# Optimization experiments

Measured on AMD Instinct MI355X. Metric: run time of the kernel, lower is better.

Reference implementation:

```python
import jax, jax.numpy as jnp
import numpy as np
import math
from jax.scipy.linalg import cho_solve

B, N, HD, H, M = 8, 2048, 512, 8, 128
VD = HD // H          # per-head dim = 64
LAM = 0.01            # lambda_noise
EPS = 0.002           # cgp_eps


def setup_inputs() -> dict:
    key = jax.random.key(0)
    ks = jax.random.split(key, 10)
    def lin(k):
        return jax.random.normal(k, (HD, HD), jnp.float32) * 0.01  # init std=0.01
    z = jnp.zeros((HD,), jnp.float32)
    return {
        "x": jax.random.normal(ks[0], (B, N, HD), jnp.float32),
        "input_mask": jnp.ones((B, N), jnp.float32),
        "Wq": lin(ks[1]), "bq": z,
        "Wk": lin(ks[2]), "bk": z,
        "Wv": lin(ks[3]), "bv": z,
        "Wx0": lin(ks[4]), "bx0": z,
        "Wo": lin(ks[5]), "bo": z,
        "omega": jax.random.normal(ks[6], (VD, M), jnp.float32),  # lengthscale=1.0
        "b_rff": 2.0 * math.pi * jax.random.uniform(ks[7], (M,), jnp.float32),
        "cur_k": 0,
    }


def _forward(x, input_mask, Wq, bq, Wk, bk, Wv, bv, Wx0, bx0, Wo, bo, omega, b_rff):
    Bb, Nn, hd = x.shape
    mask = input_mask.astype(x.dtype)
    mN = mask[:, None, :, None]                         # [B,1,N,1]

    def heads(W, bias):
        return (x @ W.T + bias).reshape(Bb, Nn, H, VD).transpose(0, 2, 1, 3)  # [B,H,N,vd]

    q = heads(Wq, bq)
    k = heads(Wk, bk)
    v = heads(Wv, bv) * mN
    x0 = heads(Wx0, bx0)

    scale = jnp.sqrt(jnp.asarray(2.0 / M, x.dtype))
    def rff(X):
        Z = jnp.einsum('bhnd,dm->bhnm', X, omega) + b_rff
        return scale * jnp.cos(Z)

    Phi_q = rff(q) * mN   # [B,H,N,m]
    Phi_k = rff(k) * mN
    Phi_o = rff(x0) * mN

    I = jnp.eye(M, dtype=x.dtype)
    Gk = jnp.einsum('bhnm,bhnp->bhmp', Phi_k, Phi_k)    # [B,H,m,m]
    Go = jnp.einsum('bhnm,bhnp->bhmp', Phi_o, Phi_o)
    Ak = Gk + LAM * I
    Ao = Go + LAM * I
    Lk = jnp.linalg.cholesky(Ak)
    Lo = jnp.linalg.cholesky(Ao)

    PkTv = jnp.einsum('bhnm,bhnd->bhmd', Phi_k, v)      # [B,H,m,vd]
    Akinv_PkTv = cho_solve((Lk, True), PkTv)
    proj = jnp.einsum('bhnm,bhmd->bhnd', Phi_k, Akinv_PkTv)
    u = (v - proj) / LAM

    Ieb = jnp.broadcast_to(I, Ao.shape)
    Ao_inv = cho_solve((Lo, True), Ieb)                 # [B,H,m,m]
    B_o = Go @ Ao_inv
    PkTu = jnp.einsum('bhnm,bhnd->bhmd', Phi_k, u)
    mid = B_o @ PkTu
    y = jnp.einsum('bhnm,bhmd->bhnd', Phi_q, mid)       # [B,H,N,vd]

    out = y.transpose(0, 2, 1, 3).reshape(Bb, Nn, hd)[:, None]  # [B,1,N,hdim]
    out = out @ Wo.T + bo

    # ---- _cgp_lower_bounds(Phi_q, Phi_k, Phi_o, v) ----
    # A = Go + lam*I == Ao (reuse Lo, Ao_inv); Ck == Gk.
    D = VD
    Cq = jnp.einsum('bhnm,bhnp->bhmp', Phi_q, Phi_q)
    Ck = Gk
    S_q = Ao / LAM + Cq / EPS
    S_k = Ao / LAM + Ck / EPS
    S_q_inv = cho_solve((jnp.linalg.cholesky(S_q), True), Ieb)
    S_k_inv = cho_solve((jnp.linalg.cholesky(S_k), True), Ieb)

    G_Ainv = Go @ Ao_inv
    const = Nn * math.log(2 * math.pi)

    # q-branch
    yy = jnp.sum(v * v, axis=(2, 3))
    PhiT_y = jnp.einsum('bhnm,bhnd->bhmd', Phi_q, v)
    Sq_inv_PhiT_y = S_q_inv @ PhiT_y
    datafit_q = yy / EPS - jnp.sum(PhiT_y * Sq_inv_PhiT_y, axis=(2, 3)) / (EPS * EPS)
    M_q = Cq / EPS - (Cq @ S_q_inv @ Cq) / (EPS * EPS)
    model_q = D * jnp.einsum('bhmn,bhmn->bh', G_Ainv, M_q)
    Iadd_q = I + (LAM / EPS) * (Ao_inv @ Cq)
    logdet_q = Nn * math.log(EPS) + jnp.linalg.slogdet(Iadd_q)[1]
    LB_q = -0.5 * (datafit_q + model_q + logdet_q + const)

    # k-branch
    tr_Ck = jnp.trace(Ck, axis1=-2, axis2=-1)
    tr_part = jnp.trace(S_k_inv @ (Ck @ Ck), axis1=-2, axis2=-1)
    datafit_k = D * (tr_Ck / EPS - tr_part / (EPS * EPS))
    M_k = Ck / EPS - (Ck @ S_k_inv @ Ck) / (EPS * EPS)
    model_k = D * jnp.einsum('bhmn,bhmn->bh', G_Ainv, M_k)
    Iadd_k = I + (LAM / EPS) * (Ao_inv @ Ck)
    logdet_k = Nn * math.log(EPS) + jnp.linalg.slogdet(Iadd_k)[1]
    LB_k = -0.5 * (datafit_k + model_k + logdet_k + const)

    reg = -(LB_q + LB_k).mean()
    return out, reg


def reference(x, input_mask, Wq, bq, Wk, bk, Wv, bv, Wx0, bx0, Wo, bo, omega, b_rff, cur_k):
    return _forward(x, input_mask, Wq, bq, Wk, bk, Wv, bv, Wx0, bx0, Wo, bo, omega, b_rff)
```

## Files before the change

### kernel.cpp

```cpp
#include <hip/hip_runtime.h>
#include <math.h>

#define B_ 8
#define N_ 2048
#define HD_ 512
#define H_ 8
#define M_ 128
#define VD_ 64

typedef __attribute__((ext_vector_type(8))) short short8v;
typedef __attribute__((ext_vector_type(4))) float f32x4;

__device__ __forceinline__ unsigned short f2bf(float f) {
  unsigned u = __float_as_uint(f);
  u += 0x7FFF + ((u >> 16) & 1);
  return (unsigned short)(u >> 16);
}
__device__ __forceinline__ float bf2f(unsigned short h) {
  return __uint_as_float(((unsigned)h) << 16);
}

__global__ __launch_bounds__(256) void split_kernel(
    const float* __restrict__ in, unsigned short* __restrict__ hi,
    unsigned short* __restrict__ lo, int n)
{
  const int i = (blockIdx.x * 256 + threadIdx.x) << 2;
  if (i >= n) return;
  float4 v = *(const float4*)(in + i);
  ushort4 h, l;
  h.x = f2bf(v.x); l.x = f2bf(v.x - bf2f(h.x));
  h.y = f2bf(v.y); l.y = f2bf(v.y - bf2f(h.y));
  h.z = f2bf(v.z); l.z = f2bf(v.z - bf2f(h.z));
  h.w = f2bf(v.w); l.w = f2bf(v.w - bf2f(h.w));
  *(ushort4*)(hi + i) = h;
  *(ushort4*)(lo + i) = l;
}

__global__ __launch_bounds__(256) void womb_kernel(
    const float* __restrict__ Wq, const float* __restrict__ Wk, const float* __restrict__ Wx0,
    const float* __restrict__ bq, const float* __restrict__ bk, const float* __restrict__ bx0,
    const float* __restrict__ omega, const float* __restrict__ brff,
    unsigned short* __restrict__ WOmH, unsigned short* __restrict__ WOmL,
    float* __restrict__ bias2)
{
  const int blk = blockIdx.x, tid = threadIdx.x;
  const int path = blk >> 10, hm = blk & 1023;
  const int h = hm >> 7, m = hm & 127;
  const float* W  = (path == 0) ? Wq : (path == 1) ? Wk : Wx0;
  const float* bv = (path == 0) ? bq : (path == 1) ? bk : bx0;
  __shared__ float om[64];
  if (tid < 64) om[tid] = omega[tid * 128 + m];
  __syncthreads();
  for (int c = tid; c < 512; c += 256) {
    float s = 0.f;
#pragma unroll 8
    for (int d = 0; d < 64; ++d) s = fmaf(W[(h * 64 + d) * 512 + c], om[d], s);
    const unsigned short sh = f2bf(s);
    const size_t o = (size_t)(path * 1024 + hm) * 512 + c;
    WOmH[o] = sh;
    WOmL[o] = f2bf(s - bf2f(sh));
  }
  if (tid == 0) {
    float s = 0.f;
    for (int d = 0; d < 64; ++d) s = fmaf(bv[h * 64 + d], om[d], s);
    bias2[path * 1024 + hm] = s + brff[m];
  }
}

#define LDP 40
#define GEMM_PROLOGUE(NCOLBITS)                                              \
  __shared__ unsigned short Ah[128 * LDP], Al[128 * LDP];                    \
  __shared__ unsigned short Bh[128 * LDP], Bl[128 * LDP];                    \
  const int tid = threadIdx.x;                                               \
  const int bx = blockIdx.x & ((1 << (NCOLBITS)) - 1);                       \
  const int by = blockIdx.x >> (NCOLBITS);                                   \
  const int row0 = by << 7, col0 = bx << 7;                                  \
  const int lane = tid & 63, wave = tid >> 6;                                \
  const int wr = wave >> 1, wc = wave & 1;                                   \
  const int fr = lane & 15, fk = (lane >> 4) << 3;                           \
  f32x4 acc[4][4];                                                           \
  _Pragma("unroll") for (int i = 0; i < 4; ++i)                              \
  _Pragma("unroll") for (int j = 0; j < 4; ++j)                              \
      acc[i][j] = (f32x4){0.f, 0.f, 0.f, 0.f};                               \
  const int srow = tid >> 2;                                                 \
  const int sch = (tid & 3) << 3;                                            \
  const size_t ga = (size_t)(row0 + srow) * 512 + sch;                       \
  const size_t gb = (size_t)(col0 + srow) * 512 + sch;                       \
  short8v rah0, rah1, ral0, ral1, rbh0, rbh1, rbl0, rbl1;

#define LOADREGS(k)                                                          \
  rah0 = *(const short8v*)(Ahi + ga + (k));                                  \
  rah1 = *(const short8v*)(Ahi + ga + (size_t)64 * 512 + (k));               \
  ral0 = *(const short8v*)(Alo + ga + (k));                                  \
  ral1 = *(const short8v*)(Alo + ga + (size_t)64 * 512 + (k));               \
  rbh0 = *(const short8v*)(Bhi + gb + (k));                                  \
  rbh1 = *(const short8v*)(Bhi + gb + (size_t)64 * 512 + (k));               \
  rbl0 = *(const short8v*)(Blo + gb + (k));                                  \
  rbl1 = *(const short8v*)(Blo + gb + (size_t)64 * 512 + (k));

#define GEMM_KLOOP                                                           \
  LOADREGS(0)                                                                \
  for (int kt = 0; kt < 16; ++kt) {                                          \
    __syncthreads();                                                         \
    *(short8v*)&Ah[srow * LDP + sch] = rah0;                                 \
    *(short8v*)&Ah[(srow + 64) * LDP + sch] = rah1;                          \
    *(short8v*)&Al[srow * LDP + sch] = ral0;                                 \
    *(short8v*)&Al[(srow + 64) * LDP + sch] = ral1;                          \
    *(short8v*)&Bh[srow * LDP + sch] = rbh0;                                 \
    *(short8v*)&Bh[(srow + 64) * LDP + sch] = rbh1;                          \
    *(short8v*)&Bl[srow * LDP + sch] = rbl0;                                 \
    *(short8v*)&Bl[(srow + 64) * LDP + sch] = rbl1;                          \
    __syncthreads();                                                         \
    if (kt < 15) { LOADREGS((kt + 1) * 32) }                                 \
    short8v a_hi[4], a_lo[4];                                                \
    _Pragma("unroll") for (int i = 0; i < 4; ++i) {                          \
      const int ar = (wr * 64 + i * 16 + fr) * LDP + fk;                     \
      a_hi[i] = *(const short8v*)&Ah[ar];                                    \
      a_lo[i] = *(const short8v*)&Al[ar];                                    \
    }                                                                        \
    _Pragma("unroll") for (int j = 0; j < 4; ++j) {                          \
      const int br = (wc * 64 + j * 16 + fr) * LDP + fk;                     \
      short8v b_hi = *(const short8v*)&Bh[br];                               \
      short8v b_lo = *(const short8v*)&Bl[br];                               \
      _Pragma("unroll") for (int i = 0; i < 4; ++i) {                        \
        acc[i][j] = __builtin_amdgcn_mfma_f32_16x16x32_bf16(a_hi[i], b_hi, acc[i][j], 0, 0, 0); \
        acc[i][j] = __builtin_amdgcn_mfma_f32_16x16x32_bf16(a_hi[i], b_lo, acc[i][j], 0, 0, 0); \
        acc[i][j] = __builtin_amdgcn_mfma_f32_16x16x32_bf16(a_lo[i], b_hi, acc[i][j], 0, 0, 0); \
      }                                                                      \
    }                                                                        \
  }

#define PT3_WRITE(HIbuf, LObuf, RBASE, NR)                                   \
  {                                                                          \
    const int hi4_ = lane >> 4;                                              \
    _Pragma("unroll") for (int j = 0; j < 4; ++j) {                          \
      const int rr = (RBASE) + wc * 64 + j * 16 + fr;                        \
      _Pragma("unroll") for (int i = 0; i < 4; ++i) {                        \
        const int npack = (n0t >> 2) + wr * 16 + hi4_ + i * 4;               \
        ushort4 hv, lv;                                                      \
        hv.x = f2bf(acc[i][j][0]); lv.x = f2bf(acc[i][j][0] - bf2f(hv.x));   \
        hv.y = f2bf(acc[i][j][1]); lv.y = f2bf(acc[i][j][1] - bf2f(hv.y));   \
        hv.z = f2bf(acc[i][j][2]); lv.z = f2bf(acc[i][j][2] - bf2f(hv.z));   \
        hv.w = f2bf(acc[i][j][3]); lv.w = f2bf(acc[i][j][3] - bf2f(hv.w));   \
        const size_t idx = ((size_t)npack * (NR) + rr) << 2;                 \
        *(ushort4*)(HIbuf + idx) = hv;                                       \
        *(ushort4*)(LObuf + idx) = lv;                                       \
      }                                                                      \
    }                                                                        \
  }

__global__ __launch_bounds__(256, 1) void gemm_out(
    const unsigned short* __restrict__ Ahi, const unsigned short* __restrict__ Alo,
    const unsigned short* __restrict__ Bhi, const unsigned short* __restrict__ Blo,
    const float* __restrict__ bias, float* __restrict__ Y)
{
  GEMM_PROLOGUE(7)
  GEMM_KLOOP
  const int hi4_ = lane >> 4;
#pragma unroll
  for (int j = 0; j < 4; ++j) {
    const int r = col0 + wc * 64 + j * 16 + fr;
#pragma unroll
    for (int i = 0; i < 4; ++i) {
      const int c0 = row0 + wr * 64 + i * 16 + (hi4_ << 2);
      const float4 bc4 = *(const float4*)(bias + c0);
      float4 o;
      o.x = acc[i][j][0] + bc4.x;
      o.y = acc[i][j][1] + bc4.y;
      o.z = acc[i][j][2] + bc4.z;
      o.w = acc[i][j][3] + bc4.w;
      *(float4*)(Y + (size_t)r * 512 + c0) = o;
    }
  }
}

__global__ __launch_bounds__(256, 1) void gemm_vt(
    const unsigned short* __restrict__ Ahi, const unsigned short* __restrict__ Alo,
    const unsigned short* __restrict__ Bhi, const unsigned short* __restrict__ Blo,
    const float* __restrict__ bias, const float* __restrict__ mask,
    unsigned short* __restrict__ VThi, unsigned short* __restrict__ VTlo)
{
  GEMM_PROLOGUE(2)
  GEMM_KLOOP
  const int b = row0 >> 11;
  const int n0t = row0 & 2047;
  const int hi4 = lane >> 4;
  float mk[4][4];
#pragma unroll
  for (int i = 0; i < 4; ++i)
#pragma unroll
    for (int r = 0; r < 4; ++r)
      mk[i][r] = mask[b * 2048 + n0t + wr * 64 + (hi4 << 2) + i * 16 + r];
#pragma unroll
  for (int j = 0; j < 4; ++j) {
    const float bc = bias[col0 + wc * 64 + j * 16 + fr];
#pragma unroll
    for (int i = 0; i < 4; ++i)
#pragma unroll
      for (int r = 0; r < 4; ++r)
        acc[i][j][r] = (acc[i][j][r] + bc) * mk[i][r];
  }
  PT3_WRITE(VThi, VTlo, b * 512 + col0, 4096)
}

__global__ __launch_bounds__(256, 1) void gemm_rff(
    const unsigned short* __restrict__ Ahi, const unsigned short* __restrict__ Alo,
    const unsigned short* __restrict__ Bhi, const unsigned short* __restrict__ Blo,
    const float* __restrict__ bias2, const float* __restrict__ mask,
    unsigned short* __restrict__ PThi, unsigned short* __restrict__ PTlo)
{
  GEMM_PROLOGUE(3)
  GEMM_KLOOP
  const int b = row0 >> 11;
  const int n0t = row0 & 2047;
  const int bh = b * 8 + bx;
  const int hi4 = lane >> 4;
  float mk[4][4];
#pragma unroll
  for (int i = 0; i < 4; ++i)
#pragma unroll
    for (int r = 0; r < 4; ++r)
      mk[i][r] = mask[b * 2048 + n0t + wr * 64 + (hi4 << 2) + i * 16 + r];
#pragma unroll
  for (int j = 0; j < 4; ++j) {
    const float bb = bias2[col0 + wc * 64 + j * 16 + fr];
#pragma unroll
    for (int i = 0; i < 4; ++i)
#pragma unroll
      for (int r = 0; r < 4; ++r)
        acc[i][j][r] = 0.125f * __cosf(acc[i][j][r] + bb) * mk[i][r];
  }
  PT3_WRITE(PThi, PTlo, bh * 128, 8192)
}

#define GPD 72
__global__ __launch_bounds__(256) void gram_ptv(
    const unsigned short* __restrict__ PThi, const unsigned short* __restrict__ PTlo,
    const unsigned short* __restrict__ VThi, const unsigned short* __restrict__ VTlo,
    float* __restrict__ GPart, float* __restrict__ PPart, int withV)
{
  __shared__ unsigned short Ath[128 * GPD], Atl[128 * GPD];
  __shared__ unsigned short Vh[64 * GPD], Vl[64 * GPD];
  const int bh = blockIdx.x, sp = blockIdx.y, tid = threadIdx.x;
  const int lane = tid & 63, wave = tid >> 6;
  const int wr = wave >> 1, wc = wave & 1;
  const int fr = lane & 15, fk = (lane >> 4) << 3;
  const int skipj = (!withV && wc == 1);
  f32x4 acc[4][6];
#pragma unroll
  for (int i = 0; i < 4; ++i)
#pragma unroll
    for (int j = 0; j < 6; ++j) acc[i][j] = (f32x4){0.f, 0.f, 0.f, 0.f};
  const int sm = tid & 127, sph = tid >> 7;
  const int sd = tid & 63, spv = tid >> 6;
  for (int n0 = sp * 512; n0 < sp * 512 + 512; n0 += 64) {
    __syncthreads();
#pragma unroll
    for (int s = 0; s < 8; ++s) {
      const int npr = sph * 8 + s;
      const size_t idx = ((size_t)((n0 >> 2) + npr) * 8192 + bh * 128 + sm) << 2;
      *(ushort4*)&Ath[sm * GPD + npr * 4] = *(const ushort4*)(PThi + idx);
      *(ushort4*)&Atl[sm * GPD + npr * 4] = *(const ushort4*)(PTlo + idx);
    }
    if (withV) {
#pragma unroll
      for (int s = 0; s < 4; ++s) {
        const int npr = spv * 4 + s;
        const size_t idx = ((size_t)((n0 >> 2) + npr) * 4096 + bh * 64 + sd) << 2;
        *(ushort4*)&Vh[sd * GPD + npr * 4] = *(const ushort4*)(VThi + idx);
        *(ushort4*)&Vl[sd * GPD + npr * 4] = *(const ushort4*)(VTlo + idx);
      }
    }
    __syncthreads();
#pragma unroll
    for (int ks = 0; ks < 2; ++ks) {
      const int ko = fk + (ks << 5);
      short8v a_h[4], a_l[4];
#pragma unroll
      for (int i = 0; i < 4; ++i) {
        const int ar = (wr * 64 + i * 16 + fr) * GPD + ko;
        a_h[i] = *(const short8v*)&Ath[ar];
        a_l[i] = *(const short8v*)&Atl[ar];
      }
#pragma unroll
      for (int j = 0; j < 6; ++j) {
        if (skipj && j >= 2) continue;
        const int c = wc * 96 + j * 16 + fr;
        short8v b_h, b_l;
        if (wc * 96 + j * 16 < 128) {
          b_h = *(const short8v*)&Ath[c * GPD + ko];
          b_l = *(const short8v*)&Atl[c * GPD + ko];
        } else {
          b_h = *(const short8v*)&Vh[(c - 128) * GPD + ko];
          b_l = *(const short8v*)&Vl[(c - 128) * GPD + ko];
        }
#pragma unroll
        for (int i = 0; i < 4; ++i) {
          acc[i][j] = __builtin_amdgcn_mfma_f32_16x16x32_bf16(a_h[i], b_h, acc[i][j], 0, 0, 0);
          acc[i][j] = __builtin_amdgcn_mfma_f32_16x16x32_bf16(a_h[i], b_l, acc[i][j], 0, 0, 0);
          acc[i][j] = __builtin_amdgcn_mfma_f32_16x16x32_bf16(a_l[i], b_h, acc[i][j], 0, 0, 0);
        }
      }
    }
  }
  const int rb = wr * 64 + ((lane >> 4) << 2);
  const size_t gob = (size_t)(sp * 64 + bh) * 16384;
  const size_t pob = (size_t)(sp * 64 + bh) * 8192;
#pragma unroll
  for (int j = 0; j < 6; ++j) {
    if (skipj && j >= 2) continue;
    const int c = wc * 96 + j * 16 + fr;
#pragma unroll
    for (int i = 0; i < 4; ++i) {
      const int m0 = rb + i * 16;
      if (wc * 96 + j * 16 < 128) {
#pragma unroll
        for (int r = 0; r < 4; ++r) GPart[gob + (size_t)(m0 + r) * 128 + c] = acc[i][j][r];
      } else {
#pragma unroll
        for (int r = 0; r < 4; ++r) PPart[pob + (size_t)(m0 + r) * 64 + (c - 128)] = acc[i][j][r];
      }
    }
  }
}

__global__ __launch_bounds__(256) void reduce4_kernel(
    const float* __restrict__ part, float* __restrict__ out, int n, size_t cs)
{
  const int i = blockIdx.x * 256 + threadIdx.x;
  if (i < n) out[i] = (part[i] + part[cs + i]) + (part[2*cs + i] + part[3*cs + i]);
}

__global__ __launch_bounds__(256) void yy_vt(
    const unsigned short* __restrict__ VThi, const unsigned short* __restrict__ VTlo,
    float* __restrict__ yyp)
{
  const int bh = blockIdx.x, ch = blockIdx.y, tid = threadIdx.x;
  float s = 0.f;
  for (int t = tid; t < 4096; t += 256) {
    const int d = t & 63, npr = t >> 6;
    const size_t idx = ((size_t)(ch * 64 + npr) * 4096 + bh * 64 + d) << 2;
    ushort4 h4 = *(const ushort4*)(VThi + idx);
    ushort4 l4 = *(const ushort4*)(VTlo + idx);
    float v;
    v = bf2f(h4.x) + bf2f(l4.x); s = fmaf(v, v, s);
    v = bf2f(h4.y) + bf2f(l4.y); s = fmaf(v, v, s);
    v = bf2f(h4.z) + bf2f(l4.z); s = fmaf(v, v, s);
    v = bf2f(h4.w) + bf2f(l4.w); s = fmaf(v, v, s);
  }
  __shared__ float red[256];
  red[tid] = s; __syncthreads();
  for (int st = 128; st > 0; st >>= 1) {
    if (tid < st) red[tid] += red[tid + st];
    __syncthreads();
  }
  if (tid == 0) yyp[ch * 64 + bh] = red[0];
}

#define ELX(i,j)  As[(((i) << 7) + ((j) ^ (((i) & 7) << 2)))]
#define EL4P(i,j4) (*(float4*)&As[(((i) << 7) + ((j4) ^ (((i) & 7) << 2)))])

__global__ __launch_bounds__(256) void chol4_kernel(
    const float* __restrict__ Gk, const float* __restrict__ Go, const float* __restrict__ Cq,
    float* __restrict__ Lk, float* __restrict__ Lo, float* __restrict__ LTq, float* __restrict__ LTk,
    float* __restrict__ ldbuf, float* __restrict__ Dinvb)
{
  __shared__ float As[128*128];
  const int bh = blockIdx.x, which = blockIdx.y, tid = threadIdx.x;
  const float* G1; const float* G2 = nullptr; float* Lout;
  if (which == 0)      { G1 = Gk; Lout = Lk;  }
  else if (which == 1) { G1 = Go; Lout = Lo;  }
  else if (which == 2) { G1 = Go; G2 = Cq; Lout = LTq; }
  else                 { G1 = Go; G2 = Gk; Lout = LTk; }
  const size_t base = (size_t)bh * 16384;
  for (int t = tid; t < 16384; t += 256) {
    float v = G1[base + t];
    if (G2) v = fmaf(5.f, G2[base + t], v);
    const int i = t >> 7, j = t & 127;
    if (i == j) v += 0.01f;
    ELX(i, j) = v;
  }
  __syncthreads();

  float ldacc = 0.f;
  for (int kb = 0; kb < 8; ++kb) {
    const int k0 = kb << 4;
    const int rbase = k0 + 16;
    const int R = 128 - rbase;
    float Dg[16][16];
    float dinv[16];
    if (tid < 128) {
#pragma unroll
      for (int j = 0; j < 16; ++j) {
#pragma unroll
        for (int p4 = 0; p4 < 16; p4 += 4) {
          float4 q = EL4P(k0 + j, k0 + p4);
          Dg[j][p4] = q.x; Dg[j][p4+1] = q.y; Dg[j][p4+2] = q.z; Dg[j][p4+3] = q.w;
        }
      }
#pragma unroll
      for (int kk = 0; kk < 16; ++kk) {
        const float d = sqrtf(Dg[kk][kk]);
        Dg[kk][kk] = d;
        const float di = 1.f / d;
        dinv[kk] = di;
#pragma unroll
        for (int r = 0; r < 16; ++r) if (r > kk) Dg[r][kk] *= di;
#pragma unroll
        for (int r = 0; r < 16; ++r) if (r > kk)
#pragma unroll
          for (int c2 = 0; c2 < 16; ++c2) if (c2 > kk && c2 <= r)
            Dg[r][c2] = fmaf(-Dg[r][kk], Dg[c2][kk], Dg[r][c2]);
      }
      if (tid == 0) {
#pragma unroll
        for (int kk = 0; kk < 16; ++kk) ldacc += logf(Dg[kk][kk]);
#pragma unroll
        for (int j = 0; j < 16; ++j) {
#pragma unroll
          for (int p4 = 0; p4 < 16; p4 += 4) {
            float4 q = {Dg[j][p4], Dg[j][p4+1], Dg[j][p4+2], Dg[j][p4+3]};
            EL4P(k0 + j, k0 + p4) = q;
          }
        }
      }
    }
    if (tid < R) {
      const int r = rbase + tid;
      float xr[16];
#pragma unroll
      for (int p4 = 0; p4 < 16; p4 += 4) {
        float4 q = EL4P(r, k0 + p4);
        xr[p4] = q.x; xr[p4+1] = q.y; xr[p4+2] = q.z; xr[p4+3] = q.w;
      }
#pragma unroll
      for (int j = 0; j < 16; ++j) {
        float s = xr[j];
#pragma unroll
        for (int p = 0; p < 16; ++p) if (p < j) s = fmaf(-Dg[j][p], xr[p], s);
        xr[j] = s * dinv[j];
      }
#pragma unroll
      for (int p4 = 0; p4 < 16; p4 += 4) {
        float4 q = {xr[p4], xr[p4+1], xr[p4+2], xr[p4+3]};
        EL4P(r, k0 + p4) = q;
      }
    }
    __syncthreads();
    if (R > 0) {
      const int Rt = R >> 2;
      const int T = (Rt * (Rt + 1)) >> 1;
      for (int idx = tid; idx < T; idx += 256) {
        int ti = (int)((sqrtf(8.f * (float)idx + 1.f) - 1.f) * 0.5f);
        while (((ti + 1) * (ti + 2)) / 2 <= idx) ++ti;
        while ((ti * (ti + 1)) / 2 > idx) --ti;
        const int tj = idx - (ti * (ti + 1)) / 2;
        const int i0 = rbase + (ti << 2), j0 = rbase + (tj << 2);
        float Li[4][16], Lj[4][16];
#pragma unroll
        for (int a = 0; a < 4; ++a)
#pragma unroll
          for (int p4 = 0; p4 < 16; p4 += 4) {
            float4 q = EL4P(i0 + a, k0 + p4);
            Li[a][p4] = q.x; Li[a][p4+1] = q.y; Li[a][p4+2] = q.z; Li[a][p4+3] = q.w;
          }
#pragma unroll
        for (int a = 0; a < 4; ++a)
#pragma unroll
          for (int p4 = 0; p4 < 16; p4 += 4) {
            float4 q = EL4P(j0 + a, k0 + p4);
            Lj[a][p4] = q.x; Lj[a][p4+1] = q.y; Lj[a][p4+2] = q.z; Lj[a][p4+3] = q.w;
          }
        float4 cc[4];
#pragma unroll
        for (int a = 0; a < 4; ++a) cc[a] = EL4P(i0 + a, j0);
#pragma unroll
        for (int p = 0; p < 16; ++p)
#pragma unroll
          for (int a = 0; a < 4; ++a) {
            cc[a].x = fmaf(-Li[a][p], Lj[0][p], cc[a].x);
            cc[a].y = fmaf(-Li[a][p], Lj[1][p], cc[a].y);
            cc[a].z = fmaf(-Li[a][p], Lj[2][p], cc[a].z);
            cc[a].w = fmaf(-Li[a][p], Lj[3][p], cc[a].w);
          }
#pragma unroll
        for (int a = 0; a < 4; ++a) EL4P(i0 + a, j0) = cc[a];
      }
    }
    __syncthreads();
  }
  for (int t = tid; t < 16384; t += 256) {
    const int i = t >> 7, j = t & 127;
    Lout[base + t] = (j <= i) ? ELX(i, j) : ELX(j, i);
  }
  if (tid < 128) Dinvb[(size_t)which * 8192 + bh * 128 + tid] = 1.f / ELX(tid, tid);
  if (tid == 0) ldbuf[which * 64 + bh] = 2.f * ldacc;
}

__global__ __launch_bounds__(256) void solve5_kernel(
    const float* __restrict__ Lk, const float* __restrict__ Lo,
    const float* __restrict__ LTq, const float* __restrict__ LTk,
    const float* __restrict__ Dinvb,
    const float* __restrict__ PkTv, const float* __restrict__ PhiTy,
    const float* __restrict__ Cq, const float* __restrict__ Gk,
    float* __restrict__ Z1, float* __restrict__ Aoi,
    float* __restrict__ Z2, float* __restrict__ Wq2, float* __restrict__ Wk2)
{
  __shared__ alignas(16) float Xs[128][128];
  __shared__ alignas(16) float Lp[128][16];
  __shared__ float di[128];
  const int bh = blockIdx.x, which = blockIdx.y, tid = threadIdx.x;
  const float* Lsrc; const float* Bsrc; float* Out; int nr; int mat;
  if (which == 0)      { Lsrc = Lk;  Bsrc = PkTv;    Out = Z1;  nr = 64;  mat = 0; }
  else if (which == 1) { Lsrc = Lo;  Bsrc = nullptr; Out = Aoi; nr = 128; mat = 1; }
  else if (which == 2) { Lsrc = LTq; Bsrc = PhiTy;   Out = Z2;  nr = 64;  mat = 2; }
  else if (which == 3) { Lsrc = LTq; Bsrc = Cq;      Out = Wq2; nr = 128; mat = 2; }
  else                 { Lsrc = LTk; Bsrc = Gk;      Out = Wk2; nr = 128; mat = 3; }
  const size_t baseL = (size_t)bh * 16384;
  const size_t baseB = (size_t)bh * 128 * (size_t)nr;
  const int sh = (nr == 64) ? 6 : 7, mk2 = nr - 1;
  if (Bsrc) {
    for (int t = tid; t < 128 * nr; t += 256) Xs[t >> sh][t & mk2] = Bsrc[baseB + t];
  } else {
    for (int t = tid; t < 16384; t += 256)
      Xs[t >> 7][t & 127] = ((t >> 7) == (t & 127)) ? 1.f : 0.f;
  }
  if (tid < 128) di[tid] = Dinvb[(size_t)mat * 8192 + bh * 128 + tid];
  const int c0 = (nr == 128) ? ((tid & 31) << 2) : ((tid & 15) << 2);
  const int rg = (nr == 128) ? (tid >> 5) : (tid >> 4);
  const int rstride = (nr == 128) ? 8 : 16;
  __syncthreads();
  for (int kb = 0; kb < 8; ++kb) {
    const int k0 = kb << 4;
    const int nrow = 128 - k0;
    for (int t = tid; t < nrow * 4; t += 256) {
      const int pr = t >> 2, pc = (t & 3) << 2;
      *(float4*)&Lp[pr][pc] = *(const float4*)(Lsrc + baseL + (size_t)(k0 + pr) * 128 + k0 + pc);
    }
    __syncthreads();
    if (tid < nr) {
      float xb[16];
#pragma unroll
      for (int j = 0; j < 16; ++j) {
        float s = Xs[k0 + j][tid];
#pragma unroll
        for (int p = 0; p < 16; ++p) if (p < j) s = fmaf(-Lp[j][p], xb[p], s);
        xb[j] = s * di[k0 + j];
        Xs[k0 + j][tid] = xb[j];
      }
    }
    __syncthreads();
    if (k0 + 16 < 128) {
      float4 xb4[16];
#pragma unroll
      for (int p = 0; p < 16; ++p) xb4[p] = *(const float4*)&Xs[k0 + p][c0];
      for (int r = k0 + 16 + rg; r < 128; r += rstride) {
        float4 xv = *(const float4*)&Xs[r][c0];
#pragma unroll
        for (int p = 0; p < 16; ++p) {
          const float l = Lp[r - k0][p];
          xv.x = fmaf(-l, xb4[p].x, xv.x);
          xv.y = fmaf(-l, xb4[p].y, xv.y);
          xv.z = fmaf(-l, xb4[p].z, xv.z);
          xv.w = fmaf(-l, xb4[p].w, xv.w);
        }
        *(float4*)&Xs[r][c0] = xv;
      }
    }
    __syncthreads();
  }
  for (int kb = 7; kb >= 0; --kb) {
    const int k0 = kb << 4;
    const int nrow = k0 + 16;
    for (int t = tid; t < nrow * 4; t += 256) {
      const int pr = t >> 2, pc = (t & 3) << 2;
      *(float4*)&Lp[pr][pc] = *(const float4*)(Lsrc + baseL + (size_t)pr * 128 + k0 + pc);
    }
    __syncthreads();
    if (tid < nr) {
      float xb[16];
#pragma unroll
      for (int j = 15; j >= 0; --j) {
        float s = Xs[k0 + j][tid];
#pragma unroll
        for (int p = 0; p < 16; ++p) if (p > j) s = fmaf(-Lp[k0 + j][p], xb[p], s);
        xb[j] = s * di[k0 + j];
        Xs[k0 + j][tid] = xb[j];
      }
    }
    __syncthreads();
    if (k0 > 0) {
      float4 xb4[16];
#pragma unroll
      for (int p = 0; p < 16; ++p) xb4[p] = *(const float4*)&Xs[k0 + p][c0];
      for (int r = rg; r < k0; r += rstride) {
        float4 xv = *(const float4*)&Xs[r][c0];
#pragma unroll
        for (int p = 0; p < 16; ++p) {
          const float l = Lp[r][p];
          xv.x = fmaf(-l, xb4[p].x, xv.x);
          xv.y = fmaf(-l, xb4[p].y, xv.y);
          xv.z = fmaf(-l, xb4[p].z, xv.z);
          xv.w = fmaf(-l, xb4[p].w, xv.w);
        }
        *(float4*)&Xs[r][c0] = xv;
      }
    }
    __syncthreads();
  }
  for (int t = tid; t < 128 * nr; t += 256) Out[baseB + t] = Xs[t >> sh][t & mk2];
}

__global__ __launch_bounds__(256) void mid_kernel(
    const float* __restrict__ Aoi, const float* __restrict__ Z1,
    float* __restrict__ midb)
{
  __shared__ alignas(16) float Ao[128][128];
  __shared__ alignas(16) float Z[128][64];
  const int bh = blockIdx.x, tid = threadIdx.x;
  const size_t bM = (size_t)bh * 16384, bD = (size_t)bh * 8192;
  for (int t4 = tid; t4 < 4096; t4 += 256) {
    const int r = t4 >> 5, c4 = (t4 & 31) << 2;
    *(float4*)&Ao[r][c4] = *(const float4*)(Aoi + bM + (size_t)r*128 + c4);
  }
  for (int t4 = tid; t4 < 2048; t4 += 256) {
    const int r = t4 >> 4, c4 = (t4 & 15) << 2;
    *(float4*)&Z[r][c4] = *(const float4*)(Z1 + bD + (size_t)r*64 + c4);
  }
  __syncthreads();
  const int ty = tid >> 4, tx = tid & 15;
  float acc[8][4];
#pragma unroll
  for (int i = 0; i < 8; ++i)
#pragma unroll
    for (int j = 0; j < 4; ++j) acc[i][j] = 0.f;
  for (int kk = 0; kk < 128; ++kk) {
    float4 a0 = *(const float4*)&Ao[kk][ty*8];
    float4 a1 = *(const float4*)&Ao[kk][ty*8+4];
    float4 bv = *(const float4*)&Z[kk][tx*4];
    float a[8] = {a0.x, a0.y, a0.z, a0.w, a1.x, a1.y, a1.z, a1.w};
    float b[4] = {bv.x, bv.y, bv.z, bv.w};
#pragma unroll
    for (int i = 0; i < 8; ++i)
#pragma unroll
      for (int j = 0; j < 4; ++j) acc[i][j] = fmaf(a[i], b[j], acc[i][j]);
  }
#pragma unroll
  for (int i = 0; i < 8; ++i) {
    const int r = ty*8 + i, c = tx*4;
    float4 o;
    o.x = Z[r][c+0] - 0.01f*acc[i][0];
    o.y = Z[r][c+1] - 0.01f*acc[i][1];
    o.z = Z[r][c+2] - 0.01f*acc[i][2];
    o.w = Z[r][c+3] - 0.01f*acc[i][3];
    *(float4*)(midb + bD + (size_t)r*64 + c) = o;
  }
}

__global__ __launch_bounds__(256) void pmat_kernel(
    const float* __restrict__ Cq, const float* __restrict__ Wq2,
    const float* __restrict__ Gk, const float* __restrict__ Wk2,
    float* __restrict__ Pq, float* __restrict__ Pk)
{
  __shared__ alignas(16) float Am[128][128];
  __shared__ alignas(16) float Bm[128][128];
  const int bh = blockIdx.x, which = blockIdx.y, tid = threadIdx.x;
  const float* Ap = which ? Gk : Cq;
  const float* Bp = which ? Wk2 : Wq2;
  float* Op = which ? Pk : Pq;
  const size_t base = (size_t)bh * 16384;
  for (int t4 = tid; t4 < 4096; t4 += 256) {
    const int r = t4 >> 5, c4 = (t4 & 31) << 2;
    *(float4*)&Am[r][c4] = *(const float4*)(Ap + base + (size_t)r*128 + c4);
    *(float4*)&Bm[r][c4] = *(const float4*)(Bp + base + (size_t)r*128 + c4);
  }
  __syncthreads();
  const int ty = tid >> 4, tx = tid & 15;
  float acc[8][8];
#pragma unroll
  for (int i = 0; i < 8; ++i)
#pragma unroll
    for (int j = 0; j < 8; ++j) acc[i][j] = 0.f;
  for (int kk = 0; kk < 128; ++kk) {
    float4 av0 = *(const float4*)&Am[kk][ty*8];
    float4 av1 = *(const float4*)&Am[kk][ty*8+4];
    float4 bv0 = *(const float4*)&Bm[kk][tx*8];
    float4 bv1 = *(const float4*)&Bm[kk][tx*8+4];
    float a[8] = {av0.x, av0.y, av0.z, av0.w, av1.x, av1.y, av1.z, av1.w};
    float b[8] = {bv0.x, bv0.y, bv0.z, bv0.w, bv1.x, bv1.y, bv1.z, bv1.w};
#pragma unroll
    for (int i = 0; i < 8; ++i)
#pragma unroll
      for (int j = 0; j < 8; ++j) acc[i][j] = fmaf(a[i], b[j], acc[i][j]);
  }
#pragma unroll
  for (int i = 0; i < 8; ++i)
#pragma unroll
    for (int j = 0; j < 8; j += 4) {
      float4 o = {acc[i][j], acc[i][j+1], acc[i][j+2], acc[i][j+3]};
      *(float4*)(Op + base + (size_t)(ty*8+i)*128 + tx*8 + j) = o;
    }
}

__global__ __launch_bounds__(256) void scalars_kernel(
    const float* __restrict__ Aoi, const float* __restrict__ Cq, const float* __restrict__ Gk,
    const float* __restrict__ Pq, const float* __restrict__ Pk, const float* __restrict__ Wk2,
    const float* __restrict__ PhiTy, const float* __restrict__ Z2,
    const float* __restrict__ yyp, const float* __restrict__ ldb,
    float* __restrict__ regp)
{
  const int bh = blockIdx.x, tid = threadIdx.x;
  const size_t b0 = (size_t)bh * 16384, b1 = (size_t)bh * 8192;
  double aoCq=0, aoGk=0, aoPq=0, aoPk=0, wkGk=0, trCq=0, trGk=0, trPq=0, trPk=0, s1=0;
  for (int t = tid; t < 16384; t += 256) {
    const double ao = Aoi[b0+t], cq = Cq[b0+t], gk = Gk[b0+t];
    const double pq = Pq[b0+t], pk = Pk[b0+t], wk = Wk2[b0+t];
    aoCq += ao*cq; aoGk += ao*gk; aoPq += ao*pq; aoPk += ao*pk; wkGk += wk*gk;
    if (t % 129 == 0) { trCq += cq; trGk += gk; trPq += pq; trPk += pk; }
  }
  for (int t = tid; t < 8192; t += 256) s1 += (double)PhiTy[b1+t] * (double)Z2[b1+t];
  __shared__ double red[256];
  double vals[10] = {aoCq, aoGk, aoPq, aoPk, wkGk, trCq, trGk, trPq, trPk, s1};
  double tot[10];
  for (int vv = 0; vv < 10; ++vv) {
    red[tid] = vals[vv];
    __syncthreads();
    for (int st = 128; st > 0; st >>= 1) {
      if (tid < st) red[tid] += red[tid+st];
      __syncthreads();
    }
    tot[vv] = red[0];
    __syncthreads();
  }
  if (tid == 0) {
    const double D = 64.0, Nd = 2048.0;
    const double ldAo = ldb[64 + bh], ldTq = ldb[128 + bh], ldTk = ldb[192 + bh];
    double yv = 0.0;
    for (int c = 0; c < 8; ++c) yv += (double)yyp[c * 64 + bh];
    const double cst  = Nd * log(2.0 * 3.14159265358979323846);
    const double leps = Nd * log(0.002);
    const double datq = 500.0*yv - 2500.0*tot[9];
    const double modq = D*(500.0*tot[5] - 2500.0*tot[7] - 0.01*(500.0*tot[0] - 2500.0*tot[2]));
    const double ldq  = leps + ldTq - ldAo;
    const double LBq  = -0.5*(datq + modq + ldq + cst);
    const double datk = D*(500.0*tot[6] - 2500.0*tot[4]);
    const double modk = D*(500.0*tot[6] - 2500.0*tot[8] - 0.01*(500.0*tot[1] - 2500.0*tot[3]));
    const double ldk  = leps + ldTk - ldAo;
    const double LBk  = -0.5*(datk + modk + ldk + cst);
    regp[bh] = (float)(-(LBq + LBk) / 64.0);
  }
}

__global__ void regfinal_kernel(const float* __restrict__ regp, float* __restrict__ outp)
{
  __shared__ float red[64];
  const int tid = threadIdx.x;
  red[tid] = regp[tid];
  __syncthreads();
  for (int st = 32; st > 0; st >>= 1) {
    if (tid < st) red[tid] += red[tid+st];
    __syncthreads();
  }
  if (tid == 0) outp[0] = red[0];
}

__global__ __launch_bounds__(256) void y_kernel(
    const unsigned short* __restrict__ PThi, const unsigned short* __restrict__ PTlo,
    const float* __restrict__ midb,
    unsigned short* __restrict__ Yhi, unsigned short* __restrict__ Ylo)
{
  __shared__ float Ps[128][129];
  __shared__ alignas(16) float Ms[128][64];
  const int blk = blockIdx.x;
  const int bh = blk >> 4, nt = blk & 15;
  const int b = bh >> 3, h = bh & 7;
  const int n0 = nt << 7;
  const int tid = threadIdx.x;
  for (int t = tid; t < 4096; t += 256) {
    const int m = t & 127, npr = t >> 7;
    const size_t idx = ((size_t)((n0 >> 2) + npr) * 8192 + bh * 128 + m) << 2;
    ushort4 h4 = *(const ushort4*)(PThi + idx);
    ushort4 l4 = *(const ushort4*)(PTlo + idx);
    Ps[npr*4+0][m] = bf2f(h4.x) + bf2f(l4.x);
    Ps[npr*4+1][m] = bf2f(h4.y) + bf2f(l4.y);
    Ps[npr*4+2][m] = bf2f(h4.z) + bf2f(l4.z);
    Ps[npr*4+3][m] = bf2f(h4.w) + bf2f(l4.w);
  }
  for (int t4 = tid; t4 < 2048; t4 += 256) {
    const int r = t4 >> 4, c4 = (t4 & 15) << 2;
    *(float4*)&Ms[r][c4] = *(const float4*)(midb + (size_t)bh*8192 + (size_t)r*64 + c4);
  }
  __syncthreads();
  const int ty = tid >> 4, tx = tid & 15;
  float acc[8][4];
#pragma unroll
  for (int i = 0; i < 8; ++i)
#pragma unroll
    for (int j = 0; j < 4; ++j) acc[i][j] = 0.f;
  for (int kk = 0; kk < 128; ++kk) {
    float4 bv = *(const float4*)&Ms[kk][tx*4];
    float b4[4] = {bv.x, bv.y, bv.z, bv.w};
#pragma unroll
    for (int i = 0; i < 8; ++i) {
      const float a = Ps[ty*8+i][kk];
      acc[i][0] = fmaf(a, b4[0], acc[i][0]);
      acc[i][1] = fmaf(a, b4[1], acc[i][1]);
      acc[i][2] = fmaf(a, b4[2], acc[i][2]);
      acc[i][3] = fmaf(a, b4[3], acc[i][3]);
    }
  }
#pragma unroll
  for (int i = 0; i < 8; ++i) {
    const size_t addr = ((size_t)(b*N_) + n0 + ty*8 + i)*512 + h*64 + tx*4;
    ushort4 hv, lv;
    hv.x = f2bf(acc[i][0]); lv.x = f2bf(acc[i][0] - bf2f(hv.x));
    hv.y = f2bf(acc[i][1]); lv.y = f2bf(acc[i][1] - bf2f(hv.y));
    hv.z = f2bf(acc[i][2]); lv.z = f2bf(acc[i][2] - bf2f(hv.z));
    hv.w = f2bf(acc[i][3]); lv.w = f2bf(acc[i][3] - bf2f(hv.w));
    *(ushort4*)(Yhi + addr) = hv;
    *(ushort4*)(Ylo + addr) = lv;
  }
}

extern "C" void kernel_launch(void* const* d_in, const int* in_sizes, int n_in,
                              void* d_out, int out_size, void* d_ws, size_t ws_size,
                              hipStream_t stream)
{
  const float* x     = (const float*)d_in[0];
  const float* mask  = (const float*)d_in[1];
  const float* Wq    = (const float*)d_in[2];
  const float* bq    = (const float*)d_in[3];
  const float* Wk    = (const float*)d_in[4];
  const float* bk    = (const float*)d_in[5];
  const float* Wv    = (const float*)d_in[6];
  const float* bv    = (const float*)d_in[7];
  const float* Wx0   = (const float*)d_in[8];
  const float* bx0   = (const float*)d_in[9];
  const float* Wo    = (const float*)d_in[10];
  const float* bo    = (const float*)d_in[11];
  const float* omega = (const float*)d_in[12];
  const float* brff  = (const float*)d_in[13];
  float* outp = (float*)d_out;

  float* W_ = (float*)d_ws;
  size_t off = 0;
  auto take = [&](size_t n) -> float* { float* p = W_ + off; off += n; return p; };
  const size_t SZ_BNH = (size_t)8*2048*512;
  const size_t SZ_MM  = (size_t)64*128*128;
  const size_t SZ_MD  = (size_t)64*128*64;

  unsigned short* Xhi  = (unsigned short*)take(SZ_BNH/2);
  unsigned short* Xlo  = (unsigned short*)take(SZ_BNH/2);
  unsigned short* PThi = (unsigned short*)take(SZ_BNH);
  unsigned short* PTlo = (unsigned short*)take(SZ_BNH);
  unsigned short* VThi = (unsigned short*)take(SZ_BNH/2);
  unsigned short* VTlo = (unsigned short*)take(SZ_BNH/2);
  unsigned short* WOmH = (unsigned short*)take(786432);
  unsigned short* WOmL = (unsigned short*)take(786432);
  float* bias2 = take(3072);
  unsigned short* WvH = (unsigned short*)take(131072);
  unsigned short* WvL = (unsigned short*)take(131072);
  unsigned short* WoH = (unsigned short*)take(131072);
  unsigned short* WoL = (unsigned short*)take(131072);
  float* Gk   = take(SZ_MM);
  float* Go   = take(SZ_MM);
  float* Cq   = take(SZ_MM);
  float* Lk   = take(SZ_MM);
  float* Lo   = take(SZ_MM);
  float* LTq  = take(SZ_MM);
  float* LTk  = take(SZ_MM);
  float* Aoi  = take(SZ_MM);
  float* Wq2  = take(SZ_MM);
  float* Wk2  = take(SZ_MM);
  float* Pq   = take(SZ_MM);
  float* Pk   = take(SZ_MM);
  float* PkTv = take(SZ_MD);
  float* PhiTy= take(SZ_MD);
  float* Z1   = take(SZ_MD);
  float* Z2   = take(SZ_MD);
  float* midb = take(SZ_MD);
  float* GPart= take(4*SZ_MM);
  float* PPart= take(4*SZ_MD);
  float* Dinv = take(4*64*128);
  float* yyp  = take(512);
  float* ldb  = take(256);
  float* regp = take(64);
  (void)ws_size; (void)in_sizes; (void)n_in; (void)out_size;

  split_kernel<<<8192, 256, 0, stream>>>(x, Xhi, Xlo, (int)SZ_BNH);
  split_kernel<<<256, 256, 0, stream>>>(Wv, WvH, WvL, 262144);
  split_kernel<<<256, 256, 0, stream>>>(Wo, WoH, WoL, 262144);
  womb_kernel<<<3072, 256, 0, stream>>>(Wq, Wk, Wx0, bq, bk, bx0, omega, brff,
                                        WOmH, WOmL, bias2);
  gemm_vt<<<512, 256, 0, stream>>>(Xhi, Xlo, WvH, WvL, bv, mask, VThi, VTlo);
  yy_vt<<<dim3(64, 8), 256, 0, stream>>>(VThi, VTlo, yyp);
  gemm_rff<<<1024, 256, 0, stream>>>(Xhi, Xlo, WOmH + 2*524288, WOmL + 2*524288,
                                     bias2 + 2048, mask, PThi, PTlo);
  gram_ptv<<<dim3(64, 4), 256, 0, stream>>>(PThi, PTlo, VThi, VTlo, GPart, PPart, 0);
  reduce4_kernel<<<4096, 256, 0, stream>>>(GPart, Go, 1048576, (size_t)1048576);
  gemm_rff<<<1024, 256, 0, stream>>>(Xhi, Xlo, WOmH + 1*524288, WOmL + 1*524288,
                                     bias2 + 1024, mask, PThi, PTlo);
  gram_ptv<<<dim3(64, 4), 256, 0, stream>>>(PThi, PTlo, VThi, VTlo, GPart, PPart, 1);
  reduce4_kernel<<<4096, 256, 0, stream>>>(GPart, Gk, 1048576, (size_t)1048576);
  reduce4_kernel<<<2048, 256, 0, stream>>>(PPart, PkTv, 524288, (size_t)524288);
  gemm_rff<<<1024, 256, 0, stream>>>(Xhi, Xlo, WOmH, WOmL,
                                     bias2, mask, PThi, PTlo);
  gram_ptv<<<dim3(64, 4), 256, 0, stream>>>(PThi, PTlo, VThi, VTlo, GPart, PPart, 1);
  reduce4_kernel<<<4096, 256, 0, stream>>>(GPart, Cq, 1048576, (size_t)1048576);
  reduce4_kernel<<<2048, 256, 0, stream>>>(PPart, PhiTy, 524288, (size_t)524288);
  chol4_kernel<<<dim3(64, 4), 256, 0, stream>>>(Gk, Go, Cq, Lk, Lo, LTq, LTk, ldb, Dinv);
  solve5_kernel<<<dim3(64, 5), 256, 0, stream>>>(Lk, Lo, LTq, LTk, Dinv, PkTv, PhiTy, Cq, Gk,
                                                 Z1, Aoi, Z2, Wq2, Wk2);
  mid_kernel<<<64, 256, 0, stream>>>(Aoi, Z1, midb);
  pmat_kernel<<<dim3(64, 2), 256, 0, stream>>>(Cq, Wq2, Gk, Wk2, Pq, Pk);
  scalars_kernel<<<64, 256, 0, stream>>>(Aoi, Cq, Gk, Pq, Pk, Wk2, PhiTy, Z2, yyp, ldb, regp);
  regfinal_kernel<<<1, 64, 0, stream>>>(regp, outp + SZ_BNH);
  y_kernel<<<1024, 256, 0, stream>>>(PThi, PTlo, midb, Xhi, Xlo);
  gemm_out<<<512, 256, 0, stream>>>(WoH, WoL, Xhi, Xlo, bo, outp);
}
```

Before: 698.7 us.

## Load GEMM tiles directly into LDS and adjust Cholesky LDS swizzle

The split-bf16 GEMM k-loop now uses global_load_lds to copy tiles straight from global memory into shared memory, dropping the register staging and the software prefetch of the next k-tile. Row padding is removed (LDP 40 to 32) to fit the contiguous layout the direct-to-LDS load expects, which may add bank conflicts on the MFMA fragment reads and loses load/compute overlap. The Cholesky kernel's shared-memory XOR swizzle is also changed to mix more row bits, meant to reduce bank conflicts.

```diff
diff --git a/kernel.cpp b/kernel.cpp
--- a/kernel.cpp
+++ b/kernel.cpp
@@ -18,6 +18,12 @@
 }
 __device__ __forceinline__ float bf2f(unsigned short h) {
   return __uint_as_float(((unsigned)h) << 16);
+}
+
+__device__ __forceinline__ void gload16(const unsigned short* g, unsigned short* l) {
+  __builtin_amdgcn_global_load_lds(
+      (const __attribute__((address_space(1))) unsigned int*)g,
+      (__attribute__((address_space(3))) unsigned int*)l, 16, 0, 0);
 }
 
 __global__ __launch_bounds__(256) void split_kernel(
@@ -67,7 +73,7 @@
   }
 }
 
-#define LDP 40
+#define LDP 32
 #define GEMM_PROLOGUE(NCOLBITS)                                              \
   __shared__ unsigned short Ah[128 * LDP], Al[128 * LDP];                    \
   __shared__ unsigned short Bh[128 * LDP], Bl[128 * LDP];                    \
@@ -86,32 +92,21 @@
   const int sch = (tid & 3) << 3;                                            \
   const size_t ga = (size_t)(row0 + srow) * 512 + sch;                       \
   const size_t gb = (size_t)(col0 + srow) * 512 + sch;                       \
-  short8v rah0, rah1, ral0, ral1, rbh0, rbh1, rbl0, rbl1;
-
-#define LOADREGS(k)                                                          \
-  rah0 = *(const short8v*)(Ahi + ga + (k));                                  \
-  rah1 = *(const short8v*)(Ahi + ga + (size_t)64 * 512 + (k));               \
-  ral0 = *(const short8v*)(Alo + ga + (k));                                  \
-  ral1 = *(const short8v*)(Alo + ga + (size_t)64 * 512 + (k));               \
-  rbh0 = *(const short8v*)(Bhi + gb + (k));                                  \
-  rbh1 = *(const short8v*)(Bhi + gb + (size_t)64 * 512 + (k));               \
-  rbl0 = *(const short8v*)(Blo + gb + (k));                                  \
-  rbl1 = *(const short8v*)(Blo + gb + (size_t)64 * 512 + (k));
+  const int ldw = wave * 512;
 
 #define GEMM_KLOOP                                                           \
-  LOADREGS(0)                                                                \
   for (int kt = 0; kt < 16; ++kt) {                                          \
+    const int kko = kt * 32;                                                 \
     __syncthreads();                                                         \
-    *(short8v*)&Ah[srow * LDP + sch] = rah0;                                 \
-    *(short8v*)&Ah[(srow + 64) * LDP + sch] = rah1;                          \
-    *(short8v*)&Al[srow * LDP + sch] = ral0;                                 \
-    *(short8v*)&Al[(srow + 64) * LDP + sch] = ral1;                          \
-    *(short8v*)&Bh[srow * LDP + sch] = rbh0;                                 \
-    *(short8v*)&Bh[(srow + 64) * LDP + sch] = rbh1;                          \
-    *(short8v*)&Bl[srow * LDP + sch] = rbl0;                                 \
-    *(short8v*)&Bl[(srow + 64) * LDP + sch] = rbl1;                          \
+    gload16(Ahi + ga + kko,                    Ah + ldw);                    \
+    gload16(Ahi + ga + (size_t)64 * 512 + kko, Ah + 64 * LDP + ldw);         \
+    gload16(Alo + ga + kko,                    Al + ldw);                    \
+    gload16(Alo + ga + (size_t)64 * 512 + kko, Al + 64 * LDP + ldw);         \
+    gload16(Bhi + gb + kko,                    Bh + ldw);                    \
+    gload16(Bhi + gb + (size_t)64 * 512 + kko, Bh + 64 * LDP + ldw);         \
+    gload16(Blo + gb + kko,                    Bl + ldw);                    \
+    gload16(Blo + gb + (size_t)64 * 512 + kko, Bl + 64 * LDP + ldw);         \
     __syncthreads();                                                         \
-    if (kt < 15) { LOADREGS((kt + 1) * 32) }                                 \
     short8v a_hi[4], a_lo[4];                                                \
     _Pragma("unroll") for (int i = 0; i < 4; ++i) {                          \
       const int ar = (wr * 64 + i * 16 + fr) * LDP + fk;                     \
@@ -357,8 +352,9 @@
   if (tid == 0) yyp[ch * 64 + bh] = red[0];
 }
 
-#define ELX(i,j)  As[(((i) << 7) + ((j) ^ (((i) & 7) << 2)))]
-#define EL4P(i,j4) (*(float4*)&As[(((i) << 7) + ((j4) ^ (((i) & 7) << 2)))])
+#define SWZ(i) ((((i) ^ ((i) >> 2)) & 7) << 2)
+#define ELX(i,j)  As[(((i) << 7) + ((j) ^ SWZ(i)))]
+#define EL4P(i,j4) (*(float4*)&As[(((i) << 7) + ((j4) ^ SWZ(i)))])
 
 __global__ __launch_bounds__(256) void chol4_kernel(
     const float* __restrict__ Gk, const float* __restrict__ Go, const float* __restrict__ Cq,
```

Result: no change. 695.4 us (median of 3 runs) (-0.5%).
